# Kernel tuning notes

Measured on AMD Instinct MI355X. Metric: run time of the kernel, lower is better.

## Reference

```python
import jax, jax.numpy as jnp
import numpy as np

NUM_CLASSES = 80
MAX_ANCHOR_MATCHES = 10
ALPHA = 0.5
BETA = 6.0
EPSILON = 1e-09
KEPS = 1e-07  # keras.backend.epsilon()
IMG = 640


def make_anchors():
    pts = []
    for stride in (8, 16, 32):
        n = IMG // stride
        xs = (jnp.arange(n, dtype=jnp.float32) + 0.5) * stride
        gy, gx = jnp.meshgrid(xs, xs, indexing='ij')
        pts.append(jnp.stack([gx.reshape(-1), gy.reshape(-1)], axis=-1))
    return jnp.concatenate(pts, axis=0)  # [8400, 2]


def make_boxes(key, shape, max_wh):
    kc, ks = jax.random.split(key)
    cxy = jax.random.uniform(kc, shape) * (IMG - 2.0 * max_wh) + max_wh
    wh = jax.random.uniform(ks, shape) * (max_wh - 4.0) + 4.0
    return jnp.concatenate([cxy - wh / 2.0, cxy + wh / 2.0], axis=-1)


def setup_inputs() -> dict:
    key = jax.random.key(0)
    B, A, C, M = 32, 8400, NUM_CLASSES, 64
    k1, k2, k3, k4 = jax.random.split(key, 4)
    scores = jax.random.uniform(k1, (B, A, C), dtype=jnp.float32)
    decode_bboxes = make_boxes(k2, (B, A, 2), 96.0)
    anchors = make_anchors()
    ground_truth_labels = jax.random.randint(k3, (B, M), 0, C, dtype=jnp.int32)
    ground_truth_bboxes = make_boxes(k4, (B, M, 2), 200.0)
    ground_truth_mask = jax.random.uniform(jax.random.fold_in(key, 7), (B, M, 1)) > 0.2
    return {
        'scores': scores,
        'decode_bboxes': decode_bboxes,
        'anchors': anchors,
        'ground_truth_labels': ground_truth_labels,
        'ground_truth_bboxes': ground_truth_bboxes,
        'ground_truth_mask': ground_truth_mask,
    }


def compute_ciou(boxes1, boxes2):
    # boxes1: [B,M,1,4], boxes2: [B,1,A,4], xyxy -> ciou [B,M,A]
    x_min1, y_min1, x_max1, y_max1 = jnp.split(boxes1, 4, axis=-1)
    x_min2, y_min2, x_max2, y_max2 = jnp.split(boxes2, 4, axis=-1)
    w1 = x_max1 - x_min1
    h1 = y_max1 - y_min1 + KEPS
    w2 = x_max2 - x_min2
    h2 = y_max2 - y_min2 + KEPS
    inter = (jnp.maximum(jnp.minimum(x_max1, x_max2) - jnp.maximum(x_min1, x_min2), 0.0)
             * jnp.maximum(jnp.minimum(y_max1, y_max2) - jnp.maximum(y_min1, y_min2), 0.0))
    union = w1 * h1 + w2 * h2 - inter + KEPS
    iou = jnp.squeeze(inter / union, -1)
    cw = jnp.maximum(x_max1, x_max2) - jnp.minimum(x_min1, x_min2)
    ch = jnp.maximum(y_max1, y_max2) - jnp.minimum(y_min1, y_min2)
    c2 = cw ** 2 + ch ** 2 + KEPS  # enclosing-box diagonal squared
    rho2 = ((x_min2 + x_max2 - x_min1 - x_max1) ** 2
            + (y_min2 + y_max2 - y_min1 - y_max1) ** 2) / 4.0  # center distance squared
    v = jnp.squeeze((4.0 / np.pi ** 2)
                    * (jnp.arctan(w2 / h2) - jnp.arctan(w1 / h1)) ** 2, -1)
    alpha = v / (v - iou + (1.0 + KEPS))
    return iou - (jnp.squeeze(rho2 / c2, -1) + v * alpha)


def reference(scores, decode_bboxes, anchors, ground_truth_labels,
              ground_truth_bboxes, ground_truth_mask):
    B, A, C = scores.shape
    M = ground_truth_bboxes.shape[1]
    K = MAX_ANCHOR_MATCHES

    # gather predicted class score for each GT label: [B, M, A]
    idx = jnp.maximum(ground_truth_labels[:, None, :], 0).astype(jnp.int32)
    bbox_scores = jnp.take_along_axis(scores, jnp.broadcast_to(idx, (B, A, M)), axis=-1)
    bbox_scores = jnp.transpose(bbox_scores, (0, 2, 1))

    overlaps = compute_ciou(ground_truth_bboxes[:, :, None, :],
                            decode_bboxes[:, None, :, :])  # [B, M, A]

    alignment = (bbox_scores ** ALPHA) * (overlaps ** BETA)
    alignment = jnp.where(ground_truth_mask, alignment, 0.0)
    in_box = jnp.all((ground_truth_bboxes[:, :, None, :2] < anchors)
                     & (ground_truth_bboxes[:, :, None, 2:] > anchors), axis=-1)
    alignment = jnp.where(in_box, alignment, 0.0)

    cand_metrics, cand_idxs = jax.lax.top_k(alignment, K)  # [B, M, K]
    cand_idxs = jnp.where(cand_metrics > 0, cand_idxs, -1)

    # sum of one-hot over K candidates == scatter-add of validity (top_k idxs distinct)
    valid = (cand_idxs >= 0).astype(overlaps.dtype)
    matched = jnp.zeros_like(overlaps).at[
        jnp.arange(B)[:, None, None],
        jnp.arange(M)[None, :, None],
        jnp.clip(cand_idxs, 0),
    ].add(valid)

    overlaps = overlaps * matched
    gt_match = jnp.argmax(overlaps, axis=1).astype(jnp.int32)  # [B, A]
    gt_match_mask = jnp.max(overlaps, axis=1) > 0

    bbox_labels = jnp.take_along_axis(
        ground_truth_bboxes, jnp.broadcast_to(gt_match[:, :, None], (B, A, 4)), axis=1)
    bbox_labels = jnp.where(gt_match_mask[:, :, None], bbox_labels, -1.0)

    class_labels = jnp.take_along_axis(ground_truth_labels, gt_match, axis=1)
    class_labels = jnp.where(gt_match_mask, class_labels, -1)
    class_onehot = jax.nn.one_hot(class_labels.astype(jnp.int32), NUM_CLASSES,
                                  dtype=scores.dtype)

    alignment = alignment * matched
    max_align = jnp.max(alignment, axis=-1, keepdims=True)  # [B, M, 1]
    max_ov = jnp.max(overlaps, axis=-1, keepdims=True)      # [B, M, 1]
    norm_align = jnp.max(alignment * max_ov / (max_align + EPSILON), axis=-2)  # [B, A]
    class_targets = class_onehot * norm_align[:, :, None]

    bbox_labels = jnp.reshape(bbox_labels, (-1, A, 4))
    return (jax.lax.stop_gradient(bbox_labels),
            jax.lax.stop_gradient(class_targets),
            jax.lax.stop_gradient((gt_match > 0).astype(jnp.float32)))
```

## Files before the change

kernel.cpp:

```cpp
#include <hip/hip_runtime.h>
#include <math.h>

#define NCLS 80
#define KTOP 10
#define NB 32
#define NA 8400
#define NM 64
#define F_EPS 1e-9f
#define F_KEPS 1e-7f
#define TPB 256
#define NSLOT 33
#define CAP 1024

__device__ __forceinline__ float ciou_one(float gx0, float gy0, float gx1, float gy1,
                                          float area1, float atanG, float4 pb)
{
    float w2 = pb.z - pb.x;
    float h2 = pb.w - pb.y + F_KEPS;
    float ix = fminf(gx1, pb.z) - fmaxf(gx0, pb.x);
    float iy = fminf(gy1, pb.w) - fmaxf(gy0, pb.y);
    float inter = fmaxf(ix, 0.f) * fmaxf(iy, 0.f);
    float uni = area1 + w2 * h2 - inter + F_KEPS;
    float iou = inter / uni;
    float cw = fmaxf(gx1, pb.z) - fminf(gx0, pb.x);
    float ch = fmaxf(gy1, pb.w) - fminf(gy0, pb.y);
    float c2 = cw * cw + ch * ch + F_KEPS;
    float dx = pb.x + pb.z - gx0 - gx1;
    float dy = pb.y + pb.w - gy0 - gy1;
    float rho2 = (dx * dx + dy * dy) * 0.25f;
    float dv = atanf(w2 / h2) - atanG;
    const float c4pi2 = 4.0f / (float)(M_PI * M_PI);
    float v = c4pi2 * dv * dv;
    float alpha = v / (v - iou + (1.0f + F_KEPS));
    return iou - (rho2 / c2 + v * alpha);
}

__global__ __launch_bounds__(256) void k_flag(const unsigned int* __restrict__ gtm_words,
                                              int* __restrict__ flag)
{
    __shared__ int s_bad;
    if (threadIdx.x == 0) s_bad = 0;
    __syncthreads();
    unsigned int w0 = gtm_words[threadIdx.x];
    unsigned int w1 = gtm_words[threadIdx.x + 256];
    if (w0 > 1u || w1 > 1u) s_bad = 1;
    __syncthreads();
    if (threadIdx.x == 0) *flag = s_bad ? 0 : 1;
}

__global__ __launch_bounds__(256) void k_align(const float* __restrict__ scores,
    const float* __restrict__ dbox, const float* __restrict__ anchors,
    const int* __restrict__ gtl, const float* __restrict__ gtb,
    const void* __restrict__ gtm, const int* __restrict__ flag,
    int* __restrict__ cand_idx, float* __restrict__ cand_ov, float* __restrict__ cand_ct)
{
    __shared__ float s_al [CAP];
    __shared__ float s_ovl[CAP];
    __shared__ int   s_pk [CAP];
    __shared__ int   s_n;
    __shared__ float s_wv[4];
    __shared__ int   s_wp[4];
    __shared__ int   s_sel[KTOP];
    __shared__ float s_selv[KTOP];
    __shared__ float s_selo[KTOP];
    __shared__ float s_ratio;

    const int bid = blockIdx.x;
    const int bm = (bid & 7) * (NB * NM / 8) + (bid >> 3);
    const int b = bm >> 6;
    const int t = threadIdx.x;

    bool maskv = (*flag) ? (((const int*)gtm)[bm] != 0)
                         : (((const unsigned char*)gtm)[bm] != 0);
    if (!maskv) {
        if (t < KTOP) {
            cand_idx[bm * KTOP + t] = -1;
            cand_ov [bm * KTOP + t] = 0.f;
            cand_ct [bm * KTOP + t] = 0.f;
        }
        return;
    }

    const float gx0 = gtb[bm * 4 + 0], gy0 = gtb[bm * 4 + 1];
    const float gx1 = gtb[bm * 4 + 2], gy1 = gtb[bm * 4 + 3];
    const int lbl = max(gtl[bm], 0);
    const float w1 = gx1 - gx0;
    const float h1 = gy1 - gy0 + F_KEPS;
    const float atanG = atanf(w1 / h1);
    const float area1 = w1 * h1;

    if (t == 0) s_n = 0;
    if (t < KTOP) { s_sel[t] = -1; s_selv[t] = 0.f; s_selo[t] = 0.f; }
    __syncthreads();

    const float4* pbv = (const float4*)dbox + (size_t)b * NA;
    const float2* anc = (const float2*)anchors;
    const float*  sb  = scores + (size_t)b * NA * NCLS + lbl;

    for (int k = 0; k < NSLOT; ++k) {
        int a = k * TPB + t;
        if (a < NA) {
            float2 an = anc[a];
            if ((gx0 < an.x) & (gy0 < an.y) & (gx1 > an.x) & (gy1 > an.y)) {
                float4 pb = pbv[a];
                float ov = ciou_one(gx0, gy0, gx1, gy1, area1, atanG, pb);
                float sc = sb[(size_t)a * NCLS];
                float t2 = ov * ov;
                float al = sqrtf(sc) * (t2 * t2 * t2);
                if (al > 0.f) {
                    int slot = atomicAdd(&s_n, 1);
                    if (slot < CAP) {
                        s_al [slot] = al;
                        s_ovl[slot] = ov;
                        s_pk [slot] = (a << 10) | slot;
                    }
                }
            }
        }
    }
    __syncthreads();
    const int n = min(s_n, CAP);

    for (int kk = 0; kk < KTOP; ++kk) {
        float bv = 0.f; int bp = 0x7fffffff;
        for (int slot = t; slot < n; slot += TPB) {
            float v = s_al[slot];
            int  pk = s_pk[slot];
            if (v > bv || (v == bv && pk < bp)) { bv = v; bp = pk; }
        }
        #pragma unroll
        for (int s = 1; s < 64; s <<= 1) {
            float qv = __shfl_xor(bv, s, 64);
            int   qp = __shfl_xor(bp, s, 64);
            if (qv > bv || (qv == bv && qp < bp)) { bv = qv; bp = qp; }
        }
        if ((t & 63) == 0) { s_wv[t >> 6] = bv; s_wp[t >> 6] = bp; }
        __syncthreads();
        float wv = s_wv[0]; int wp = s_wp[0];
        #pragma unroll
        for (int w = 1; w < 4; ++w) {
            float v2 = s_wv[w]; int p2 = s_wp[w];
            if (v2 > wv || (v2 == wv && p2 < wp)) { wv = v2; wp = p2; }
        }
        __syncthreads();
        if (wv <= 0.f) break;
        if (t == 0) {
            int slot = wp & (CAP - 1);
            s_sel [kk] = wp >> 10;
            s_selv[kk] = wv;
            s_selo[kk] = s_ovl[slot];
            s_al[slot] = -1.f;
        }
        __syncthreads();
    }
    __syncthreads();

    if (t == 0) {
        float max_al = s_selv[0];
        float max_ov = 0.f;
        for (int k2 = 0; k2 < KTOP; ++k2)
            if (s_sel[k2] >= 0) max_ov = fmaxf(max_ov, s_selo[k2]);
        s_ratio = max_ov / (max_al + F_EPS);
    }
    __syncthreads();
    if (t < KTOP) {
        int id = s_sel[t];
        cand_idx[bm * KTOP + t] = id;
        cand_ov [bm * KTOP + t] = (id >= 0) ? s_selo[t] : 0.f;
        cand_ct [bm * KTOP + t] = (id >= 0) ? s_selv[t] * s_ratio : 0.f;
    }
}

__global__ __launch_bounds__(256) void k_out(const float* __restrict__ gtb,
    const int* __restrict__ gtl,
    const int* __restrict__ cand_idx, const float* __restrict__ cand_ov,
    const float* __restrict__ cand_ct,
    float* __restrict__ out_bbox, float* __restrict__ out_cls,
    float* __restrict__ out_match)
{
    __shared__ int   s_idx[NM * KTOP];
    __shared__ float s_ov [NM * KTOP];
    __shared__ float s_ct [NM * KTOP];
    const int b = blockIdx.y;
    const int a0 = blockIdx.x * 256;
    const int t = threadIdx.x;
    const int a = a0 + t;

    for (int i = t; i < NM * KTOP; i += 256) {
        s_idx[i] = cand_idx[b * NM * KTOP + i];
        s_ov [i] = cand_ov [b * NM * KTOP + i];
        s_ct [i] = cand_ct [b * NM * KTOP + i];
    }

    const int nA = min(256, NA - a0);
    float4* cb = (float4*)(out_cls + ((size_t)b * NA + a0) * NCLS);
    const int nW = nA * NCLS / 4;
    for (int i = t; i < nW; i += 256) cb[i] = make_float4(0.f, 0.f, 0.f, 0.f);

    __syncthreads();

    if (a < NA) {
        unsigned long long mm = 0ull;
        float best_v = -INFINITY; int best_m = NM;
        float normv = 0.f;
        for (int m = 0; m < NM; ++m) {
            #pragma unroll
            for (int k = 0; k < KTOP; ++k) {
                int id = s_idx[m * KTOP + k];
                if (id == a) {
                    mm |= (1ull << m);
                    float v = s_ov[m * KTOP + k];
                    if (v > best_v) { best_v = v; best_m = m; }
                    normv = fmaxf(normv, s_ct[m * KTOP + k]);
                }
            }
        }
        unsigned long long inv = ~mm;
        int mz = (inv == 0ull) ? NM : __builtin_ctzll(inv);
        float wv; int wm;
        if (mz < NM) { wv = 0.f; wm = mz; } else { wv = -INFINITY; wm = 0; }
        if (mm != 0ull && (best_v > wv || (best_v == wv && best_m < wm))) {
            wv = best_v; wm = best_m;
        }
        bool matched = wv > 0.f;

        float4 bb = matched ? ((const float4*)gtb)[b * NM + wm]
                            : make_float4(-1.f, -1.f, -1.f, -1.f);
        ((float4*)out_bbox)[(size_t)b * NA + a] = bb;
        out_match[(size_t)b * NA + a] = (wm > 0) ? 1.f : 0.f;
        if (matched) {
            int c = gtl[b * NM + wm];
            if ((unsigned)c < NCLS)
                out_cls[((size_t)b * NA + a) * NCLS + c] = normv;
        }
    }
}

extern "C" void kernel_launch(void* const* d_in, const int* in_sizes, int n_in,
                              void* d_out, int out_size, void* d_ws, size_t ws_size,
                              hipStream_t stream)
{
    const float* scores  = (const float*)d_in[0];
    const float* dbox    = (const float*)d_in[1];
    const float* anchors = (const float*)d_in[2];
    const int*   gtl     = (const int*)d_in[3];
    const float* gtb     = (const float*)d_in[4];
    const void*  gtm     = d_in[5];

    char* ws = (char*)d_ws;
    int*   flag  = (int*)ws;
    char* p = ws + 16;
    int*   cand_idx = (int*)p;    p += (size_t)NB * NM * KTOP * 4;
    float* cand_ov  = (float*)p;  p += (size_t)NB * NM * KTOP * 4;
    float* cand_ct  = (float*)p;

    float* out_bbox  = (float*)d_out;
    float* out_cls   = out_bbox + (size_t)NB * NA * 4;
    float* out_match = out_cls + (size_t)NB * NA * NCLS;

    k_flag<<<1, 256, 0, stream>>>((const unsigned int*)gtm, flag);
    k_align<<<NB * NM, 256, 0, stream>>>(
        scores, dbox, anchors, gtl, gtb, gtm, flag,
        cand_idx, cand_ov, cand_ct);
    k_out<<<dim3((NA + 255) / 256, NB), 256, 0, stream>>>(
        gtb, gtl, cand_idx, cand_ov, cand_ct, out_bbox, out_cls, out_match);
}
```

Baseline: 230.1 us.

## Fold mask-type detection into align kernel, warp-aggregate atomics, prefilter candidates per block

Removes the separate single-block flag kernel: every align block now reads the mask words itself to decide whether the mask is int or byte. This saves a launch and a serial dependency but adds redundant global reads in each block. Candidate slot allocation now uses a ballot and one shared atomic per wavefront instead of one atomic per lane. The output kernel first compacts only the candidates that fall inside its 256-anchor range, so each thread scans a short list instead of all 640 entries.

```diff
diff --git a/kernel.cpp b/kernel.cpp
--- a/kernel.cpp
+++ b/kernel.cpp
@@ -11,6 +11,7 @@
 #define TPB 256
 #define NSLOT 33
 #define CAP 1024
+#define NCAND (NM * KTOP)
 
 __device__ __forceinline__ float ciou_one(float gx0, float gy0, float gx1, float gy1,
                                           float area1, float atanG, float4 pb)
@@ -35,29 +36,17 @@
     return iou - (rho2 / c2 + v * alpha);
 }
 
-__global__ __launch_bounds__(256) void k_flag(const unsigned int* __restrict__ gtm_words,
-                                              int* __restrict__ flag)
-{
-    __shared__ int s_bad;
-    if (threadIdx.x == 0) s_bad = 0;
-    __syncthreads();
-    unsigned int w0 = gtm_words[threadIdx.x];
-    unsigned int w1 = gtm_words[threadIdx.x + 256];
-    if (w0 > 1u || w1 > 1u) s_bad = 1;
-    __syncthreads();
-    if (threadIdx.x == 0) *flag = s_bad ? 0 : 1;
-}
-
 __global__ __launch_bounds__(256) void k_align(const float* __restrict__ scores,
     const float* __restrict__ dbox, const float* __restrict__ anchors,
     const int* __restrict__ gtl, const float* __restrict__ gtb,
-    const void* __restrict__ gtm, const int* __restrict__ flag,
+    const void* __restrict__ gtm,
     int* __restrict__ cand_idx, float* __restrict__ cand_ov, float* __restrict__ cand_ct)
 {
     __shared__ float s_al [CAP];
     __shared__ float s_ovl[CAP];
     __shared__ int   s_pk [CAP];
     __shared__ int   s_n;
+    __shared__ int   s_bad;
     __shared__ float s_wv[4];
     __shared__ int   s_wp[4];
     __shared__ int   s_sel[KTOP];
@@ -69,9 +58,22 @@
     const int bm = (bid & 7) * (NB * NM / 8) + (bid >> 3);
     const int b = bm >> 6;
     const int t = threadIdx.x;
-
-    bool maskv = (*flag) ? (((const int*)gtm)[bm] != 0)
-                         : (((const unsigned char*)gtm)[bm] != 0);
+    const int lane = t & 63;
+
+    if (t == 0) { s_bad = 0; s_n = 0; }
+    __syncthreads();
+    {
+        const unsigned int* gw = (const unsigned int*)gtm;
+        unsigned int w0 = gw[t];
+        unsigned int w1 = gw[t + 256];
+        if (w0 > 1u || w1 > 1u) s_bad = 1;
+    }
+    if (t < KTOP) { s_sel[t] = -1; s_selv[t] = 0.f; s_selo[t] = 0.f; }
+    __syncthreads();
+    const bool int_mask = (s_bad == 0);
+
+    bool maskv = int_mask ? (((const int*)gtm)[bm] != 0)
+                          : (((const unsigned char*)gtm)[bm] != 0);
     if (!maskv) {
         if (t < KTOP) {
             cand_idx[bm * KTOP + t] = -1;
@@ -89,31 +91,38 @@
     const float atanG = atanf(w1 / h1);
     const float area1 = w1 * h1;
 
-    if (t == 0) s_n = 0;
-    if (t < KTOP) { s_sel[t] = -1; s_selv[t] = 0.f; s_selo[t] = 0.f; }
-    __syncthreads();
-
     const float4* pbv = (const float4*)dbox + (size_t)b * NA;
     const float2* anc = (const float2*)anchors;
     const float*  sb  = scores + (size_t)b * NA * NCLS + lbl;
 
     for (int k = 0; k < NSLOT; ++k) {
         int a = k * TPB + t;
+        float al = 0.f, ov = 0.f;
         if (a < NA) {
             float2 an = anc[a];
             if ((gx0 < an.x) & (gy0 < an.y) & (gx1 > an.x) & (gy1 > an.y)) {
                 float4 pb = pbv[a];
-                float ov = ciou_one(gx0, gy0, gx1, gy1, area1, atanG, pb);
+                ov = ciou_one(gx0, gy0, gx1, gy1, area1, atanG, pb);
                 float sc = sb[(size_t)a * NCLS];
                 float t2 = ov * ov;
-                float al = sqrtf(sc) * (t2 * t2 * t2);
-                if (al > 0.f) {
-                    int slot = atomicAdd(&s_n, 1);
-                    if (slot < CAP) {
-                        s_al [slot] = al;
-                        s_ovl[slot] = ov;
-                        s_pk [slot] = (a << 10) | slot;
-                    }
+                al = sqrtf(sc) * (t2 * t2 * t2);
+            }
+        }
+        bool pos = al > 0.f;
+        unsigned long long ball = __ballot(pos);
+        if (ball) {
+            int leader = (int)__builtin_ctzll(ball);
+            int cnt = __popcll(ball);
+            int base = 0;
+            if (lane == leader) base = atomicAdd(&s_n, cnt);
+            base = __shfl(base, leader, 64);
+            if (pos) {
+                int rank = __popcll(ball & ((1ull << lane) - 1ull));
+                int slot = base + rank;
+                if (slot < CAP) {
+                    s_al [slot] = al;
+                    s_ovl[slot] = ov;
+                    s_pk [slot] = (a << 10) | slot;
                 }
             }
         }
@@ -134,7 +143,7 @@
             int   qp = __shfl_xor(bp, s, 64);
             if (qv > bv || (qv == bv && qp < bp)) { bv = qv; bp = qp; }
         }
-        if ((t & 63) == 0) { s_wv[t >> 6] = bv; s_wp[t >> 6] = bp; }
+        if (lane == 0) { s_wv[t >> 6] = bv; s_wp[t >> 6] = bp; }
         __syncthreads();
         float wv = s_wv[0]; int wp = s_wp[0];
         #pragma unroll
@@ -178,18 +187,27 @@
     float* __restrict__ out_bbox, float* __restrict__ out_cls,
     float* __restrict__ out_match)
 {
-    __shared__ int   s_idx[NM * KTOP];
-    __shared__ float s_ov [NM * KTOP];
-    __shared__ float s_ct [NM * KTOP];
+    __shared__ int   s_fpk[NCAND];
+    __shared__ float s_fov[NCAND];
+    __shared__ float s_fct[NCAND];
+    __shared__ int   s_fn;
     const int b = blockIdx.y;
     const int a0 = blockIdx.x * 256;
     const int t = threadIdx.x;
     const int a = a0 + t;
 
-    for (int i = t; i < NM * KTOP; i += 256) {
-        s_idx[i] = cand_idx[b * NM * KTOP + i];
-        s_ov [i] = cand_ov [b * NM * KTOP + i];
-        s_ct [i] = cand_ct [b * NM * KTOP + i];
+    if (t == 0) s_fn = 0;
+    __syncthreads();
+
+    for (int i = t; i < NCAND; i += 256) {
+        int id = cand_idx[b * NCAND + i];
+        unsigned int d = (unsigned int)(id - a0);
+        if (d < 256u) {
+            int slot = atomicAdd(&s_fn, 1);
+            s_fpk[slot] = ((int)d << 6) | (i / KTOP);
+            s_fov[slot] = cand_ov[b * NCAND + i];
+            s_fct[slot] = cand_ct[b * NCAND + i];
+        }
     }
 
     const int nA = min(256, NA - a0);
@@ -198,25 +216,24 @@
     for (int i = t; i < nW; i += 256) cb[i] = make_float4(0.f, 0.f, 0.f, 0.f);
 
     __syncthreads();
+    const int fn = s_fn;
 
     if (a < NA) {
         unsigned long long mm = 0ull;
         float best_v = -INFINITY; int best_m = NM;
         float normv = 0.f;
-        for (int m = 0; m < NM; ++m) {
-            #pragma unroll
-            for (int k = 0; k < KTOP; ++k) {
-                int id = s_idx[m * KTOP + k];
-                if (id == a) {
-                    mm |= (1ull << m);
-                    float v = s_ov[m * KTOP + k];
-                    if (v > best_v) { best_v = v; best_m = m; }
-                    normv = fmaxf(normv, s_ct[m * KTOP + k]);
-                }
+        for (int i = 0; i < fn; ++i) {
+            int pk = s_fpk[i];
+            if ((pk >> 6) == t) {
+                int m = pk & 63;
+                mm |= (1ull << m);
+                float v = s_fov[i];
+                if (v > best_v || (v == best_v && m < best_m)) { best_v = v; best_m = m; }
+                normv = fmaxf(normv, s_fct[i]);
             }
         }
         unsigned long long inv = ~mm;
-        int mz = (inv == 0ull) ? NM : __builtin_ctzll(inv);
+        int mz = (inv == 0ull) ? NM : (int)__builtin_ctzll(inv);
         float wv; int wm;
         if (mz < NM) { wv = 0.f; wm = mz; } else { wv = -INFINITY; wm = 0; }
         if (mm != 0ull && (best_v > wv || (best_v == wv && best_m < wm))) {
@@ -247,20 +264,17 @@
     const float* gtb     = (const float*)d_in[4];
     const void*  gtm     = d_in[5];
 
-    char* ws = (char*)d_ws;
-    int*   flag  = (int*)ws;
-    char* p = ws + 16;
-    int*   cand_idx = (int*)p;    p += (size_t)NB * NM * KTOP * 4;
-    float* cand_ov  = (float*)p;  p += (size_t)NB * NM * KTOP * 4;
+    char* p = (char*)d_ws;
+    int*   cand_idx = (int*)p;    p += (size_t)NB * NCAND * 4;
+    float* cand_ov  = (float*)p;  p += (size_t)NB * NCAND * 4;
     float* cand_ct  = (float*)p;
 
     float* out_bbox  = (float*)d_out;
     float* out_cls   = out_bbox + (size_t)NB * NA * 4;
     float* out_match = out_cls + (size_t)NB * NA * NCLS;
 
-    k_flag<<<1, 256, 0, stream>>>((const unsigned int*)gtm, flag);
     k_align<<<NB * NM, 256, 0, stream>>>(
-        scores, dbox, anchors, gtl, gtb, gtm, flag,
+        scores, dbox, anchors, gtl, gtb, gtm,
         cand_idx, cand_ov, cand_ct);
     k_out<<<dim3((NA + 255) / 256, NB), 256, 0, stream>>>(
         gtb, gtl, cand_idx, cand_ov, cand_ct, out_bbox, out_cls, out_match);
```

Result: faster. 204.5 us (-11.1%).
